# Kernel tuning notes

Measured on AMD Instinct MI355X. Metric: run time of the kernel, lower is better.

Reference implementation:

```python
import math
import jax, jax.numpy as jnp
import numpy as np

B, L, D_IN, H, NLAYER, FUT, MDIM = 16, 128, 8, 128, 2, 12, 2

def setup_inputs() -> dict:
    key = jax.random.key(0)
    ks = jax.random.split(key, 16)
    def rn(k, shape, scale=0.05):
        return jax.random.normal(k, shape, jnp.float32) * scale
    return {
        'history': jax.random.normal(ks[0], (B, L, D_IN), jnp.float32),
        'history_mask': jnp.ones((B, L), jnp.float32),
        'Wp': rn(ks[1], (D_IN, H)), 'bp': jnp.zeros((H,), jnp.float32),
        'We1': rn(ks[2], (NLAYER, 4, H)), 'be1': jnp.zeros((NLAYER, H), jnp.float32),
        'We2': rn(ks[3], (NLAYER, H, H)), 'be2': jnp.zeros((NLAYER, H), jnp.float32),
        'Wa1': rn(ks[4], (NLAYER, 3 * H, H)), 'ba1': jnp.zeros((NLAYER, H), jnp.float32),
        'wa2': rn(ks[5], (NLAYER, H)), 'ba2': jnp.zeros((NLAYER,), jnp.float32),
        'Wm1': rn(ks[6], (NLAYER, 2 * H, H)), 'bm1': jnp.zeros((NLAYER, H), jnp.float32),
        'Wm2': rn(ks[7], (NLAYER, H, H)), 'bm2': jnp.zeros((NLAYER, H), jnp.float32),
        'Wo1': rn(ks[8], (NLAYER, 2 * H, H)), 'bo1': jnp.zeros((NLAYER, H), jnp.float32),
        'Wo2': rn(ks[9], (NLAYER, H, H)), 'bo2': jnp.zeros((NLAYER, H), jnp.float32),
        'ln_g': jnp.ones((NLAYER, H), jnp.float32), 'ln_b': jnp.zeros((NLAYER, H), jnp.float32),
        'hg': jnp.ones((D_IN + H,), jnp.float32), 'hb': jnp.zeros((D_IN + H,), jnp.float32),
        'Wh1': rn(ks[10], (D_IN + H, H)), 'bh1': jnp.zeros((H,), jnp.float32),
        'Wh2': rn(ks[11], (H, FUT * MDIM)), 'bh2': jnp.zeros((FUT * MDIM,), jnp.float32),
    }

def _layer_norm(x, g, b):
    mu = jnp.mean(x, -1, keepdims=True)
    var = jnp.mean((x - mu) ** 2, -1, keepdims=True)
    return (x - mu) * jax.lax.rsqrt(var + 1e-5) * g + b

def _forward(history, history_mask, Wp, bp, We1, be1, We2, be2, Wa1, ba1, wa2, ba2,
             Wm1, bm1, Wm2, bm2, Wo1, bo1, Wo2, bo2, ln_g, ln_b, hg, hb, Wh1, bh1, Wh2, bh2):
    valid = history_mask > 0
    vm = valid.astype(jnp.float32)[..., None]
    ts = jnp.cumsum(jnp.maximum(history[..., 5], 0.0), axis=1)
    # edge features [B,L,L,4]: dist, dt/300, same_src, same_step
    lat, lon, src_flag = history[..., 0], history[..., 1], history[..., 6]
    dlat = lat[:, :, None] - lat[:, None, :]
    dlon = lon[:, :, None] - lon[:, None, :]
    dist = jnp.sqrt(dlat * dlat + dlon * dlon + 1e-8)
    dt = jnp.abs(ts[:, :, None] - ts[:, None, :]) / 300.0
    same_src = (src_flag[:, :, None] == src_flag[:, None, :]).astype(jnp.float32)
    same_step = jnp.broadcast_to(jnp.eye(L, dtype=jnp.float32), (B, L, L))
    edge_feat = jnp.stack([dist, dt, same_src, same_step], axis=-1)
    h = (history @ Wp + bp) * vm
    inv = 1.0 / math.sqrt(H)
    for l in range(NLAYER):
        eh = jax.nn.relu(edge_feat @ We1[l] + be1[l]) @ We2[l] + be2[l]  # [B,L,L,H]
        # att MLP on concat([src,dst,edge]) -> split first weight into blocks
        sa = h @ Wa1[l, :H]       # src term, varies over i
        da = h @ Wa1[l, H:2 * H]  # dst term, varies over j
        att_hid = jnp.tanh(sa[:, :, None, :] + da[:, None, :, :] + eh @ Wa1[l, 2 * H:] + ba1[l])
        att = (att_hid @ wa2[l] + ba2[l]) * inv  # [B,L,L]
        att = jnp.where(valid[:, None, :], att, -1e9)  # key invalid
        att = jnp.where(valid[:, :, None], att, -1e9)  # query invalid
        w = jax.nn.softmax(att, axis=-1)
        # msg MLP on concat([src, edge])
        msg = jax.nn.relu((h @ Wm1[l, :H])[:, :, None, :] + eh @ Wm1[l, H:] + bm1[l]) @ Wm2[l] + bm2[l]
        agg = jnp.einsum('bij,bijk->bik', w, msg)
        out = jax.nn.relu(h @ Wo1[l, :H] + agg @ Wo1[l, H:] + bo1[l]) @ Wo2[l] + bo2[l]
        h = _layer_norm(h + out, ln_g[l], ln_b[l]) * vm
    # decoder state: last valid step
    vc = jnp.clip(jnp.sum(history_mask, axis=1).astype(jnp.int32), 1, L)
    last = vc - 1
    bidx = jnp.arange(B)
    ds = jnp.concatenate([history[bidx, last], h[bidx, last]], axis=-1)
    x = _layer_norm(ds, hg, hb)
    pred = (jax.nn.relu(x @ Wh1 + bh1) @ Wh2 + bh2).reshape(B, FUT, MDIM)
    pred = jnp.nan_to_num(pred, nan=0.0, posinf=1e4, neginf=-1e4)
    return pred, h

def reference(history, history_mask, Wp, bp, We1, be1, We2, be2, Wa1, ba1, wa2, ba2,
              Wm1, bm1, Wm2, bm2, Wo1, bo1, Wo2, bo2, ln_g, ln_b, hg, hb, Wh1, bh1, Wh2, bh2):
    return _forward(history, history_mask, Wp, bp, We1, be1, We2, be2, Wa1, ba1, wa2, ba2,
                    Wm1, bm1, Wm2, bm2, Wo1, bo1, Wo2, bo2, ln_g, ln_b, hg, hb, Wh1, bh1, Wh2, bh2)
```

## Files before the change

### kernel.cpp

```cpp
#include <hip/hip_runtime.h>
#include <math.h>

#define BB 16
#define LL 128
#define D_IN 8
#define HH 128
#define NLAYER 2
#define FUT 12
#define MDIM 2

typedef __attribute__((ext_vector_type(8))) __bf16 bf16x8;
typedef __attribute__((ext_vector_type(8))) short short8v;
typedef __attribute__((ext_vector_type(4))) float f32x4;

#define MFMA_B16(A, B, C) __builtin_amdgcn_mfma_f32_16x16x32_bf16(A, B, C, 0, 0, 0)

static __device__ __forceinline__ short f2bf(float f) {
    union { float f; unsigned u; } v; v.f = f;
    unsigned r = v.u + 0x7FFFu + ((v.u >> 16) & 1u);
    return (short)(r >> 16);
}

static __device__ __forceinline__ float tanh_fast(float x) {
    float e = __expf(2.f * x);
    return 1.f - 2.f / (e + 1.f);
}

__global__ __launch_bounds__(256) void k_prep(const float* __restrict__ hist, const float* __restrict__ mask,
                                              const float* __restrict__ Wp, const float* __restrict__ bp,
                                              const float* __restrict__ We2, const float* __restrict__ be2,
                                              const float* __restrict__ Wa1, const float* __restrict__ ba1,
                                              const float* __restrict__ Wm1, const float* __restrict__ bm1,
                                              const float* __restrict__ Wo1, const float* __restrict__ Wm2,
                                              const float* __restrict__ Wo2,
                                              float* __restrict__ ts, float* __restrict__ h,
                                              short* __restrict__ AmT, short* __restrict__ MmT,
                                              float* __restrict__ ca, float* __restrict__ cm,
                                              short* __restrict__ WT4, short* __restrict__ WT3) {
    __shared__ float row[HH];
    __shared__ float pa[256], pm[256];
    const int bid = blockIdx.x, tid = threadIdx.x;
    const int NC = NLAYER * (HH + 1);
    if (bid < BB) {
        int b = bid;
        if (tid < LL) row[tid] = fmaxf(hist[(b * LL + tid) * D_IN + 5], 0.f);
        __syncthreads();
        for (int d = 1; d < LL; d <<= 1) {
            float add = (tid < LL && tid >= d) ? row[tid - d] : 0.f;
            __syncthreads();
            if (tid < LL) row[tid] += add;
            __syncthreads();
        }
        if (tid < LL) ts[b * LL + tid] = row[tid];
        int k = tid & (HH - 1);
        float wp_r[D_IN];
#pragma unroll
        for (int f = 0; f < D_IN; f++) wp_r[f] = Wp[f * HH + k];
        float bpk = bp[k];
        int jbase = tid >> 7;
        for (int e = 0; e < 64; e++) {
            int j = e * 2 + jbase;
            int bj = b * LL + j;
            const float* hr = hist + (size_t)bj * D_IN;
            float acc = bpk;
#pragma unroll
            for (int f = 0; f < D_IN; f++) acc += hr[f] * wp_r[f];
            h[(size_t)bj * HH + k] = acc * (mask[bj] > 0.f ? 1.f : 0.f);
        }
    } else if (bid < BB + NC) {
        int cb = bid - BB;
        int l = cb / (HH + 1);
        int p = cb % (HH + 1);
        const float* WaE = Wa1 + (size_t)(l * 3 * HH + 2 * HH) * HH;
        const float* WmE = Wm1 + (size_t)(l * 2 * HH + HH) * HH;
        int q = tid & 127, kh = tid >> 7;
        if (tid < HH) row[tid] = (p < HH) ? We2[(size_t)(l * HH + p) * HH + tid] : be2[l * HH + tid];
        __syncthreads();
        float a = 0.f, m = 0.f;
        int kbase = kh * 64;
#pragma unroll 4
        for (int k = 0; k < 64; k++) {
            float w = row[kbase + k];
            a += w * WaE[(size_t)(kbase + k) * HH + q];
            m += w * WmE[(size_t)(kbase + k) * HH + q];
        }
        pa[tid] = a;
        pm[tid] = m;
        __syncthreads();
        if (tid < HH) {
            a = pa[tid] + pa[128 + tid];
            m = pm[tid] + pm[128 + tid];
            if (p < HH) {
                AmT[(size_t)l * HH * HH + tid * HH + p] = f2bf(a);
                MmT[(size_t)l * HH * HH + tid * HH + p] = f2bf(m);
            } else {
                ca[l * HH + tid] = a + ba1[l * HH + tid];
                cm[l * HH + tid] = m + bm1[l * HH + tid];
            }
        }
    } else {
        int m7 = bid - BB - NC;
        int l = m7 / 7, m = m7 % 7;
        const float* src;
        switch (m) {
            case 0: src = Wa1 + (size_t)(l * 3 * HH) * HH; break;
            case 1: src = Wa1 + (size_t)(l * 3 * HH + HH) * HH; break;
            case 2: src = Wm1 + (size_t)(l * 2 * HH) * HH; break;
            case 3: src = Wo1 + (size_t)(l * 2 * HH) * HH; break;
            case 4: src = Wm2 + (size_t)l * HH * HH; break;
            case 5: src = Wo1 + (size_t)(l * 2 * HH + HH) * HH; break;
            default: src = Wo2 + (size_t)l * HH * HH; break;
        }
        short* dst = (m < 4) ? (WT4 + (size_t)(l * 4 + m) * HH * HH)
                             : (WT3 + (size_t)(l * 3 + (m - 4)) * HH * HH);
#pragma unroll 4
        for (int e = 0; e < 64; e++) {
            int idx = e * 256 + tid;
            int kk = idx >> 7;
            int c = idx & 127;
            dst[c * HH + kk] = f2bf(src[(size_t)kk * HH + c]);
        }
    }
}

__global__ __launch_bounds__(256) void k_pre(const float* __restrict__ h, const short* __restrict__ WT4,
                                             const float* __restrict__ ca, const float* __restrict__ cm,
                                             float* __restrict__ base_a, float* __restrict__ da,
                                             float* __restrict__ base_m, float* __restrict__ oa, int l) {
    __shared__ __align__(16) short hA[16][136];
    const int tid = threadIdx.x, lane = tid & 63, wv = tid >> 6;
    const int lo = lane & 15, g4 = lane >> 4;
    const int rt = blockIdx.x >> 1, half = blockIdx.x & 1;
    const int r0 = rt * 16;
    {
        int row = tid >> 4, cc = (tid & 15) * 8;
        const float* hr = h + (size_t)(r0 + row) * HH + cc;
        short8v pk;
#pragma unroll
        for (int e = 0; e < 8; e++) pk[e] = f2bf(hr[e]);
        *(short8v*)&hA[row][cc] = pk;
    }
    __syncthreads();
    bf16x8 af[4];
#pragma unroll
    for (int ks = 0; ks < 4; ks++)
        af[ks] = *(const bf16x8*)&hA[lo][ks * 32 + g4 * 8];
    const int mat = half * 2 + (wv & 1);
    const int ctbase = (wv >> 1) * 4;
    const short* Wl = WT4 + (size_t)(l * 4 + mat) * HH * HH;
    float* dst;
    const float* bias = nullptr;
    if (mat == 0) { dst = base_a; bias = ca + l * HH; }
    else if (mat == 1) dst = da;
    else if (mat == 2) { dst = base_m; bias = cm + l * HH; }
    else dst = oa;
#pragma unroll
    for (int cc2 = 0; cc2 < 4; cc2++) {
        int col = (ctbase + cc2) * 16 + lo;
        bf16x8 Bf[4];
#pragma unroll
        for (int ks = 0; ks < 4; ks++)
            Bf[ks] = *(const bf16x8*)(Wl + (size_t)col * HH + ks * 32 + g4 * 8);
        f32x4 acc = (f32x4){0.f, 0.f, 0.f, 0.f};
#pragma unroll
        for (int ks = 0; ks < 4; ks++) acc = MFMA_B16(af[ks], Bf[ks], acc);
        float bv = bias ? bias[col] : 0.f;
#pragma unroll
        for (int rg = 0; rg < 4; rg++)
            dst[(size_t)(r0 + g4 * 4 + rg) * HH + col] = acc[rg] + bv;
    }
}

__global__ __launch_bounds__(512) void k_attn(
    const float* __restrict__ hist, const float* __restrict__ mask, const float* __restrict__ ts,
    const float* __restrict__ base_a_g, const float* __restrict__ base_m_g, const float* __restrict__ da,
    const short* __restrict__ AmT, const short* __restrict__ MmT,
    const float* __restrict__ wa2, const float* __restrict__ ba2,
    const float* __restrict__ We1, const float* __restrict__ be1,
    float* __restrict__ v_out, int l) {
    __shared__ __align__(16) short t_lds[LL][LL];
    __shared__ __align__(16) float bufA[1024];
    __shared__ float w_lds[LL];
    __shared__ float val_s[LL];

    const int tid = threadIdx.x;
    const int lane = tid & 63;
    const int wv = tid >> 6;
    const int lo = lane & 15, g4 = lane >> 4;
    const int kq = wv * 16 + g4 * 4;
    const int bi = blockIdx.x, b = bi >> 7, i = bi & (LL - 1);

    const f32x4 ba4 = *(const f32x4*)(base_a_g + (size_t)bi * HH + kq);
    const f32x4 bm4 = *(const f32x4*)(base_m_g + (size_t)bi * HH + kq);
    const f32x4 wa4 = *(const f32x4*)(wa2 + l * HH + kq);
    const float ba2l = ba2[l];

    bf16x8 Bf[4];
#pragma unroll
    for (int ks = 0; ks < 4; ks++)
        Bf[ks] = *(const bf16x8*)(AmT + (size_t)l * HH * HH + (size_t)(wv * 16 + lo) * HH + ks * 32 + g4 * 8);

    {
        const float* We1l = We1 + l * 4 * HH;
        const float* be1l = be1 + l * HH;
        if (tid < 256) bufA[tid] = We1l[tid];
        else if (tid < 384) bufA[tid] = be1l[tid - 256];
        else bufA[tid] = be1l[tid - 384] + We1l[256 + (tid - 384)];
        if (tid < 128) {
            bufA[512 + tid] = We1l[384 + tid];
            val_s[tid] = mask[b * LL + tid];
        }
    }
    __syncthreads();

    {
        int jj = tid & (LL - 1);
        int q4 = tid >> 7;
        const float* hri = hist + (size_t)(b * LL + i) * D_IN;
        const float* hrj = hist + (size_t)(b * LL + jj) * D_IN;
        float dlat = hri[0] - hrj[0], dlon = hri[1] - hrj[1];
        float ea = sqrtf(dlat * dlat + dlon * dlon + 1e-8f);
        float eb = fabsf(ts[b * LL + i] - ts[b * LL + jj]) * (1.f / 300.f);
        const float* basep = bufA + ((hri[6] == hrj[6]) ? 384 : 256);
        char* trow = (char*)t_lds + jj * 256;
        int swz = (jj & 7) << 4;
        bool diag = (jj == i);
#pragma unroll
        for (int pass = 0; pass < 4; pass++) {
            int r0c = (q4 + pass * 4) * 8;
            f32x4 v0, v1;
            {
                f32x4 wa0 = *(const f32x4*)&bufA[r0c];
                f32x4 wb0 = *(const f32x4*)&bufA[128 + r0c];
                f32x4 bs0 = *(const f32x4*)&basep[r0c];
                v0 = wa0 * ea + wb0 * eb + bs0;
                f32x4 wa1 = *(const f32x4*)&bufA[r0c + 4];
                f32x4 wb1 = *(const f32x4*)&bufA[128 + r0c + 4];
                f32x4 bs1 = *(const f32x4*)&basep[r0c + 4];
                v1 = wa1 * ea + wb1 * eb + bs1;
            }
            if (diag) {
                v0 += *(const f32x4*)&bufA[512 + r0c];
                v1 += *(const f32x4*)&bufA[512 + r0c + 4];
            }
            bf16x8 pkb;
#pragma unroll
            for (int e = 0; e < 4; e++) {
                pkb[e] = (__bf16)fmaxf(v0[e], 0.f);
                pkb[4 + e] = (__bf16)fmaxf(v1[e], 0.f);
            }
            *(bf16x8*)(trow + ((r0c * 2) ^ swz)) = pkb;
        }
    }
    __syncthreads();

    const float* da_b = da + (size_t)(b * LL) * HH;
    const int rswz = (lo & 7) << 4;

#pragma unroll
    for (int jh = 0; jh < 2; jh++) {
        f32x4 acc[4];
#pragma unroll
        for (int m = 0; m < 4; m++) {
            int j0 = (jh * 4 + m) * 16 + lo;
            acc[m] = *(const f32x4*)(da_b + (size_t)j0 * HH + kq);
        }
#pragma unroll
        for (int ks = 0; ks < 4; ks++) {
            bf16x8 tf[4];
#pragma unroll
            for (int m = 0; m < 4; m++) {
                int row = (jh * 4 + m) * 16 + lo;
                tf[m] = *(const bf16x8*)((const char*)t_lds + row * 256 + ((ks * 64 + g4 * 16) ^ rswz));
            }
#pragma unroll
            for (int m = 0; m < 4; m++) acc[m] = MFMA_B16(Bf[ks], tf[m], acc[m]);
        }
#pragma unroll
        for (int m = 0; m < 4; m++) {
            f32x4 s = acc[m] + ba4;
            float p0 = tanh_fast(s[0]) * wa4[0];
            float p1 = tanh_fast(s[1]) * wa4[1];
            float p2 = tanh_fast(s[2]) * wa4[2];
            float p3 = tanh_fast(s[3]) * wa4[3];
            float p = (p0 + p1) + (p2 + p3);
            p += __shfl_xor(p, 16);
            p += __shfl_xor(p, 32);
            if (g4 == 0) bufA[wv * LL + (jh * 4 + m) * 16 + lo] = p;
        }
    }

#pragma unroll
    for (int ks = 0; ks < 4; ks++)
        Bf[ks] = *(const bf16x8*)(MmT + (size_t)l * HH * HH + (size_t)(wv * 16 + lo) * HH + ks * 32 + g4 * 8);
    __syncthreads();

    {
        const float inv = 0.08838834764831845f;
        float vi = val_s[i];
        float a0 = ba2l, a1 = ba2l;
#pragma unroll
        for (int w = 0; w < 8; w++) {
            a0 += bufA[w * LL + lane];
            a1 += bufA[w * LL + 64 + lane];
        }
        a0 *= inv; a1 *= inv;
        if (!(val_s[lane] > 0.f) || !(vi > 0.f)) a0 = -1e9f;
        if (!(val_s[64 + lane] > 0.f) || !(vi > 0.f)) a1 = -1e9f;
        float m = fmaxf(a0, a1);
#pragma unroll
        for (int d = 1; d < 64; d <<= 1) m = fmaxf(m, __shfl_xor(m, d));
        float e0 = __expf(a0 - m), e1 = __expf(a1 - m);
        float s = e0 + e1;
#pragma unroll
        for (int d = 1; d < 64; d <<= 1) s += __shfl_xor(s, d);
        float rs = 1.f / s;
        w_lds[lane] = e0 * rs;
        w_lds[64 + lane] = e1 * rs;
    }

    f32x4 macv = (f32x4){0.f, 0.f, 0.f, 0.f};
#pragma unroll
    for (int jh = 0; jh < 2; jh++) {
        f32x4 acc[4];
#pragma unroll
        for (int m = 0; m < 4; m++) acc[m] = (f32x4){0.f, 0.f, 0.f, 0.f};
#pragma unroll
        for (int ks = 0; ks < 4; ks++) {
            bf16x8 tf[4];
#pragma unroll
            for (int m = 0; m < 4; m++) {
                int row = (jh * 4 + m) * 16 + lo;
                tf[m] = *(const bf16x8*)((const char*)t_lds + row * 256 + ((ks * 64 + g4 * 16) ^ rswz));
            }
#pragma unroll
            for (int m = 0; m < 4; m++) acc[m] = MFMA_B16(Bf[ks], tf[m], acc[m]);
        }
#pragma unroll
        for (int m = 0; m < 4; m++) {
            float wj = w_lds[(jh * 4 + m) * 16 + lo];
            f32x4 mm = acc[m] + bm4;
#pragma unroll
            for (int rg = 0; rg < 4; rg++) mm[rg] = fmaxf(mm[rg], 0.f);
            macv += mm * wj;
        }
    }
#pragma unroll
    for (int rg = 0; rg < 4; rg++) {
        macv[rg] += __shfl_xor(macv[rg], 1);
        macv[rg] += __shfl_xor(macv[rg], 2);
        macv[rg] += __shfl_xor(macv[rg], 4);
        macv[rg] += __shfl_xor(macv[rg], 8);
    }
    if (lo == 0) *(f32x4*)(v_out + (size_t)bi * HH + kq) = macv;
}

__global__ __launch_bounds__(256) void k_post(
    const float* __restrict__ v, const float* __restrict__ oa_in, const float* __restrict__ h,
    const float* __restrict__ mask, const short* __restrict__ WT3,
    const float* __restrict__ bm2, const float* __restrict__ bo1, const float* __restrict__ bo2,
    const float* __restrict__ ln_g, const float* __restrict__ ln_b,
    float* __restrict__ hout, float* __restrict__ hcopy, int l,
    int do_pre, const short* __restrict__ WT4, const float* __restrict__ ca, const float* __restrict__ cm,
    float* __restrict__ base_a, float* __restrict__ da, float* __restrict__ base_m, float* __restrict__ oa_out,
    const float* __restrict__ hist, const float* __restrict__ hg, const float* __restrict__ hb,
    const float* __restrict__ Wh1, const float* __restrict__ bh1,
    const float* __restrict__ Wh2, const float* __restrict__ bh2, float* __restrict__ dec_out) {
    __shared__ __align__(16) short xA[16][136];
    __shared__ __align__(16) short iA[16][136];
    __shared__ float red[2][4][16];
    __shared__ float ln_row[HH];
    __shared__ float dec_x[D_IN + HH];
    const int tid = threadIdx.x, lane = tid & 63, wv = tid >> 6;
    const int lo = lane & 15, g4 = lane >> 4;
    const int r0 = blockIdx.x * 16;

    float oaR[2][4], hR[2][4], vmR[4];
    float bm2R[2], bo1R[2], bo2R[2], gR[2], bR[2];
#pragma unroll
    for (int ct = 0; ct < 2; ct++) {
        int c = wv * 32 + ct * 16 + lo;
        bm2R[ct] = bm2[l * HH + c];
        bo1R[ct] = bo1[l * HH + c];
        bo2R[ct] = bo2[l * HH + c];
        gR[ct] = ln_g[l * HH + c];
        bR[ct] = ln_b[l * HH + c];
    }
#pragma unroll
    for (int rg = 0; rg < 4; rg++) {
        int r = r0 + g4 * 4 + rg;
        vmR[rg] = mask[r];
#pragma unroll
        for (int ct = 0; ct < 2; ct++) {
            int c = wv * 32 + ct * 16 + lo;
            oaR[ct][rg] = oa_in[(size_t)r * HH + c];
            hR[ct][rg] = h[(size_t)r * HH + c];
        }
    }

    int lastRow = -1;
    if (hcopy) {
        float mv = (tid < LL) ? mask[(r0 >> 7) * LL + tid] : 0.f;
#pragma unroll
        for (int d = 1; d < 64; d <<= 1) mv += __shfl_xor(mv, d);
        if (lane == 0) red[0][wv][0] = mv;
    }

    {
        int row = tid >> 4, cc = (tid & 15) * 8;
        const float* vr = v + (size_t)(r0 + row) * HH + cc;
        short8v pk;
#pragma unroll
        for (int e = 0; e < 8; e++) pk[e] = f2bf(vr[e]);
        *(short8v*)&xA[row][cc] = pk;
    }
    __syncthreads();

    if (hcopy) {
        int vc = (int)(red[0][0][0] + red[0][1][0] + red[0][2][0] + red[0][3][0]);
        vc = min(max(vc, 1), LL);
        lastRow = (r0 & ~(LL - 1)) + vc - 1;
    }

    bf16x8 af[4], Bf[2][4];
    f32x4 acc[2];

    {
        const short* W = WT3 + (size_t)(l * 3 + 0) * HH * HH;
#pragma unroll
        for (int ks = 0; ks < 4; ks++) af[ks] = *(const bf16x8*)&xA[lo][ks * 32 + g4 * 8];
#pragma unroll
        for (int ct = 0; ct < 2; ct++) {
            int col = wv * 32 + ct * 16 + lo;
#pragma unroll
            for (int ks = 0; ks < 4; ks++)
                Bf[ct][ks] = *(const bf16x8*)(W + (size_t)col * HH + ks * 32 + g4 * 8);
        }
        acc[0] = (f32x4){0.f, 0.f, 0.f, 0.f};
        acc[1] = (f32x4){0.f, 0.f, 0.f, 0.f};
#pragma unroll
        for (int ks = 0; ks < 4; ks++) {
            acc[0] = MFMA_B16(af[ks], Bf[0][ks], acc[0]);
            acc[1] = MFMA_B16(af[ks], Bf[1][ks], acc[1]);
        }
#pragma unroll
        for (int ct = 0; ct < 2; ct++)
#pragma unroll
            for (int rg = 0; rg < 4; rg++)
                iA[g4 * 4 + rg][wv * 32 + ct * 16 + lo] = f2bf(acc[ct][rg] + bm2R[ct]);
    }
    __syncthreads();

    {
        const short* W = WT3 + (size_t)(l * 3 + 1) * HH * HH;
#pragma unroll
        for (int ks = 0; ks < 4; ks++) af[ks] = *(const bf16x8*)&iA[lo][ks * 32 + g4 * 8];
#pragma unroll
        for (int ct = 0; ct < 2; ct++) {
            int col = wv * 32 + ct * 16 + lo;
#pragma unroll
            for (int ks = 0; ks < 4; ks++)
                Bf[ct][ks] = *(const bf16x8*)(W + (size_t)col * HH + ks * 32 + g4 * 8);
        }
        acc[0] = (f32x4){0.f, 0.f, 0.f, 0.f};
        acc[1] = (f32x4){0.f, 0.f, 0.f, 0.f};
#pragma unroll
        for (int ks = 0; ks < 4; ks++) {
            acc[0] = MFMA_B16(af[ks], Bf[0][ks], acc[0]);
            acc[1] = MFMA_B16(af[ks], Bf[1][ks], acc[1]);
        }
        __syncthreads();
#pragma unroll
        for (int ct = 0; ct < 2; ct++)
#pragma unroll
            for (int rg = 0; rg < 4; rg++)
                xA[g4 * 4 + rg][wv * 32 + ct * 16 + lo] =
                    f2bf(fmaxf(acc[ct][rg] + oaR[ct][rg] + bo1R[ct], 0.f));
    }
    __syncthreads();

    float y[2][4];
    {
        const short* W = WT3 + (size_t)(l * 3 + 2) * HH * HH;
#pragma unroll
        for (int ks = 0; ks < 4; ks++) af[ks] = *(const bf16x8*)&xA[lo][ks * 32 + g4 * 8];
#pragma unroll
        for (int ct = 0; ct < 2; ct++) {
            int col = wv * 32 + ct * 16 + lo;
#pragma unroll
            for (int ks = 0; ks < 4; ks++)
                Bf[ct][ks] = *(const bf16x8*)(W + (size_t)col * HH + ks * 32 + g4 * 8);
        }
        acc[0] = (f32x4){0.f, 0.f, 0.f, 0.f};
        acc[1] = (f32x4){0.f, 0.f, 0.f, 0.f};
#pragma unroll
        for (int ks = 0; ks < 4; ks++) {
            acc[0] = MFMA_B16(af[ks], Bf[0][ks], acc[0]);
            acc[1] = MFMA_B16(af[ks], Bf[1][ks], acc[1]);
        }
#pragma unroll
        for (int ct = 0; ct < 2; ct++)
#pragma unroll
            for (int rg = 0; rg < 4; rg++)
                y[ct][rg] = acc[ct][rg] + bo2R[ct] + hR[ct][rg];
    }
#pragma unroll
    for (int rg = 0; rg < 4; rg++) {
        float s = y[0][rg] + y[1][rg];
        float s2 = y[0][rg] * y[0][rg] + y[1][rg] * y[1][rg];
#pragma unroll
        for (int d = 1; d < 16; d <<= 1) { s += __shfl_xor(s, d); s2 += __shfl_xor(s2, d); }
        if (lo == 0) {
            red[0][wv][g4 * 4 + rg] = s;
            red[1][wv][g4 * 4 + rg] = s2;
        }
    }
    __syncthreads();
#pragma unroll
    for (int rg = 0; rg < 4; rg++) {
        int rl = g4 * 4 + rg;
        float mu = (red[0][0][rl] + red[0][1][rl] + red[0][2][rl] + red[0][3][rl]) * (1.f / HH);
        float ex2 = (red[1][0][rl] + red[1][1][rl] + red[1][2][rl] + red[1][3][rl]) * (1.f / HH);
        float var = ex2 - mu * mu;
        float rs = rsqrtf(var + 1e-5f);
        float vm = vmR[rg] > 0.f ? 1.f : 0.f;
        int r = r0 + rl;
#pragma unroll
        for (int ct = 0; ct < 2; ct++) {
            int c = wv * 32 + ct * 16 + lo;
            float hv = ((y[ct][rg] - mu) * rs * gR[ct] + bR[ct]) * vm;
            hout[(size_t)r * HH + c] = hv;
            if (hcopy) hcopy[(size_t)r * HH + c] = hv;
            if (do_pre) xA[rl][c] = f2bf(hv);
            if (lastRow >= 0 && r == lastRow) ln_row[c] = hv;
        }
    }

    if (do_pre) {
        __syncthreads();
        bf16x8 af2[4];
#pragma unroll
        for (int ks = 0; ks < 4; ks++) af2[ks] = *(const bf16x8*)&xA[lo][ks * 32 + g4 * 8];
        int ln = l + 1;
        const short* Wl = WT4 + (size_t)(ln * 4 + wv) * HH * HH;
        float* dst;
        const float* bias = nullptr;
        if (wv == 0) { dst = base_a; bias = ca + ln * HH; }
        else if (wv == 1) dst = da;
        else if (wv == 2) { dst = base_m; bias = cm + ln * HH; }
        else dst = oa_out;
#pragma unroll
        for (int ct = 0; ct < 8; ct++) {
            int col = ct * 16 + lo;
            bf16x8 Bf2[4];
#pragma unroll
            for (int ks = 0; ks < 4; ks++)
                Bf2[ks] = *(const bf16x8*)(Wl + (size_t)col * HH + ks * 32 + g4 * 8);
            f32x4 a2 = (f32x4){0.f, 0.f, 0.f, 0.f};
#pragma unroll
            for (int ks = 0; ks < 4; ks++) a2 = MFMA_B16(af2[ks], Bf2[ks], a2);
            float bv = bias ? bias[col] : 0.f;
#pragma unroll
            for (int rg = 0; rg < 4; rg++)
                dst[(size_t)(r0 + g4 * 4 + rg) * HH + col] = a2[rg] + bv;
        }
    }

    if (hcopy && lastRow >= r0 && lastRow < r0 + 16) {
        const int N = D_IN + HH;
        __syncthreads();
        if (tid < D_IN) dec_x[tid] = hist[(size_t)lastRow * D_IN + tid];
        if (tid < HH) dec_x[D_IN + tid] = ln_row[tid];
        __syncthreads();
        float px = (tid < N) ? dec_x[tid] : 0.f;
        float px2 = px * px;
#pragma unroll
        for (int d = 1; d < 64; d <<= 1) { px += __shfl_xor(px, d); px2 += __shfl_xor(px2, d); }
        if (lane == 0) { red[0][wv][0] = px; red[1][wv][0] = px2; }
        __syncthreads();
        float mu = (red[0][0][0] + red[0][1][0] + red[0][2][0] + red[0][3][0]) / (float)N;
        float ex2 = (red[1][0][0] + red[1][1][0] + red[1][2][0] + red[1][3][0]) / (float)N;
        float var = ex2 - mu * mu;
        float rs = rsqrtf(var + 1e-5f);
        if (tid < N) dec_x[tid] = (dec_x[tid] - mu) * rs * hg[tid] + hb[tid];
        __syncthreads();
        if (tid < HH) {
            float a = bh1[tid];
            for (int f = 0; f < N; f++) a += dec_x[f] * Wh1[(size_t)f * HH + tid];
            ln_row[tid] = fmaxf(a, 0.f);
        }
        __syncthreads();
        if (tid < FUT * MDIM) {
            float o = bh2[tid];
            for (int k = 0; k < HH; k++) o += ln_row[k] * Wh2[(size_t)k * FUT * MDIM + tid];
            if (isnan(o)) o = 0.f;
            else if (isinf(o)) o = (o > 0.f) ? 1e4f : -1e4f;
            dec_out[(r0 >> 7) * FUT * MDIM + tid] = o;
        }
    }
}

extern "C" void kernel_launch(void* const* d_in, const int* in_sizes, int n_in,
                              void* d_out, int out_size, void* d_ws, size_t ws_size,
                              hipStream_t stream) {
    const float* hist = (const float*)d_in[0];
    const float* mask = (const float*)d_in[1];
    const float* Wp  = (const float*)d_in[2];
    const float* bp  = (const float*)d_in[3];
    const float* We1 = (const float*)d_in[4];
    const float* be1 = (const float*)d_in[5];
    const float* We2 = (const float*)d_in[6];
    const float* be2 = (const float*)d_in[7];
    const float* Wa1 = (const float*)d_in[8];
    const float* ba1 = (const float*)d_in[9];
    const float* wa2 = (const float*)d_in[10];
    const float* ba2 = (const float*)d_in[11];
    const float* Wm1 = (const float*)d_in[12];
    const float* bm1 = (const float*)d_in[13];
    const float* Wm2 = (const float*)d_in[14];
    const float* bm2 = (const float*)d_in[15];
    const float* Wo1 = (const float*)d_in[16];
    const float* bo1 = (const float*)d_in[17];
    const float* Wo2 = (const float*)d_in[18];
    const float* bo2 = (const float*)d_in[19];
    const float* ln_g = (const float*)d_in[20];
    const float* ln_b = (const float*)d_in[21];
    const float* hg  = (const float*)d_in[22];
    const float* hb  = (const float*)d_in[23];
    const float* Wh1 = (const float*)d_in[24];
    const float* bh1 = (const float*)d_in[25];
    const float* Wh2 = (const float*)d_in[26];
    const float* bh2 = (const float*)d_in[27];
    float* out = (float*)d_out;

    float* ws = (float*)d_ws;
    float* ts_w   = ws; ws += BB * LL;
    float* h_w    = ws; ws += BB * LL * HH;
    float* da_w   = ws; ws += BB * LL * HH;
    float* ba_w   = ws; ws += BB * LL * HH;
    float* bm_w   = ws; ws += BB * LL * HH;
    float* oa_w   = ws; ws += BB * LL * HH;
    float* v_w    = ws; ws += BB * LL * HH;
    float* ca_w   = ws; ws += NLAYER * HH;
    float* cm_w   = ws; ws += NLAYER * HH;
    short* AmT_w  = (short*)ws; ws += NLAYER * HH * HH / 2;
    short* MmT_w  = (short*)ws; ws += NLAYER * HH * HH / 2;
    short* WT4_w  = (short*)ws; ws += NLAYER * 4 * HH * HH / 2;
    short* WT3_w  = (short*)ws; ws += NLAYER * 3 * HH * HH / 2;

    const int NPREP = BB + NLAYER * (HH + 1) + NLAYER * 7;
    k_prep<<<NPREP, 256, 0, stream>>>(hist, mask, Wp, bp, We2, be2, Wa1, ba1, Wm1, bm1,
                                      Wo1, Wm2, Wo2, ts_w, h_w, AmT_w, MmT_w, ca_w, cm_w, WT4_w, WT3_w);
    k_pre<<<BB * LL / 16 * 2, 256, 0, stream>>>(h_w, WT4_w, ca_w, cm_w, ba_w, da_w, bm_w, oa_w, 0);
    for (int l = 0; l < NLAYER; l++) {
        k_attn<<<BB * LL, 512, 0, stream>>>(hist, mask, ts_w, ba_w, bm_w, da_w, AmT_w, MmT_w,
                                            wa2, ba2, We1, be1, v_w, l);
        int do_pre = (l < NLAYER - 1) ? 1 : 0;
        float* hcopy = (l == NLAYER - 1) ? (out + BB * FUT * MDIM) : nullptr;
        k_post<<<BB * LL / 16, 256, 0, stream>>>(v_w, oa_w, h_w, mask, WT3_w, bm2, bo1, bo2,
                                                 ln_g, ln_b, h_w, hcopy, l,
                                                 do_pre, WT4_w, ca_w, cm_w, ba_w, da_w, bm_w, oa_w,
                                                 hist, hg, hb, Wh1, bh1, Wh2, bh2, out);
    }
}
```

Before: 258.5 us.

## Widen k_pre and k_post to 512 threads and prefetch weight fragments

k_pre and k_post now run 8 waves per 16-row block instead of 4, with each wave owning one 16-column tile (k_post) or one matrix half (k_pre). All B-fragments are loaded from global memory up front, before the LDS staging and barriers, so the weight loads overlap them. k_prep stages the history rows and mask in shared memory instead of re-reading global memory inside the loop. The cost is higher register pressure from holding all weight fragments, plus larger cross-wave reductions for the layer norm.

```diff
diff --git a/kernel.cpp b/kernel.cpp
--- a/kernel.cpp
+++ b/kernel.cpp
@@ -11,6 +11,7 @@
 
 typedef __attribute__((ext_vector_type(8))) __bf16 bf16x8;
 typedef __attribute__((ext_vector_type(8))) short short8v;
+typedef __attribute__((ext_vector_type(4))) short short4v;
 typedef __attribute__((ext_vector_type(4))) float f32x4;
 
 #define MFMA_B16(A, B, C) __builtin_amdgcn_mfma_f32_16x16x32_bf16(A, B, C, 0, 0, 0)
@@ -39,11 +40,16 @@
                                               short* __restrict__ WT4, short* __restrict__ WT3) {
     __shared__ float row[HH];
     __shared__ float pa[256], pm[256];
+    __shared__ float hrow[LL * D_IN];
     const int bid = blockIdx.x, tid = threadIdx.x;
     const int NC = NLAYER * (HH + 1);
     if (bid < BB) {
         int b = bid;
-        if (tid < LL) row[tid] = fmaxf(hist[(b * LL + tid) * D_IN + 5], 0.f);
+#pragma unroll
+        for (int e = 0; e < 4; e++) hrow[e * 256 + tid] = hist[(size_t)b * LL * D_IN + e * 256 + tid];
+        if (tid < LL) pa[tid] = mask[b * LL + tid];
+        __syncthreads();
+        if (tid < LL) row[tid] = fmaxf(hrow[tid * D_IN + 5], 0.f);
         __syncthreads();
         for (int d = 1; d < LL; d <<= 1) {
             float add = (tid < LL && tid >= d) ? row[tid - d] : 0.f;
@@ -60,12 +66,11 @@
         int jbase = tid >> 7;
         for (int e = 0; e < 64; e++) {
             int j = e * 2 + jbase;
-            int bj = b * LL + j;
-            const float* hr = hist + (size_t)bj * D_IN;
+            const float* hr = &hrow[j * D_IN];
             float acc = bpk;
 #pragma unroll
             for (int f = 0; f < D_IN; f++) acc += hr[f] * wp_r[f];
-            h[(size_t)bj * HH + k] = acc * (mask[bj] > 0.f ? 1.f : 0.f);
+            h[(size_t)(b * LL + j) * HH + k] = acc * (pa[j] > 0.f ? 1.f : 0.f);
         }
     } else if (bid < BB + NC) {
         int cb = bid - BB;
@@ -123,31 +128,39 @@
     }
 }
 
-__global__ __launch_bounds__(256) void k_pre(const float* __restrict__ h, const short* __restrict__ WT4,
+__global__ __launch_bounds__(512) void k_pre(const float* __restrict__ h, const short* __restrict__ WT4,
                                              const float* __restrict__ ca, const float* __restrict__ cm,
                                              float* __restrict__ base_a, float* __restrict__ da,
                                              float* __restrict__ base_m, float* __restrict__ oa, int l) {
     __shared__ __align__(16) short hA[16][136];
     const int tid = threadIdx.x, lane = tid & 63, wv = tid >> 6;
     const int lo = lane & 15, g4 = lane >> 4;
-    const int rt = blockIdx.x >> 1, half = blockIdx.x & 1;
-    const int r0 = rt * 16;
+    const int r0 = blockIdx.x * 16;
+    const int mat = wv >> 1, colh = wv & 1;
+
+    const short* Wl = WT4 + (size_t)(l * 4 + mat) * HH * HH;
+    bf16x8 Bf[4][4];
+#pragma unroll
+    for (int t = 0; t < 4; t++) {
+        int col = (colh * 4 + t) * 16 + lo;
+#pragma unroll
+        for (int ks = 0; ks < 4; ks++)
+            Bf[t][ks] = *(const bf16x8*)(Wl + (size_t)col * HH + ks * 32 + g4 * 8);
+    }
+
     {
-        int row = tid >> 4, cc = (tid & 15) * 8;
+        int row = tid >> 5, cc = (tid & 31) * 4;
         const float* hr = h + (size_t)(r0 + row) * HH + cc;
-        short8v pk;
-#pragma unroll
-        for (int e = 0; e < 8; e++) pk[e] = f2bf(hr[e]);
-        *(short8v*)&hA[row][cc] = pk;
+        short4v pk;
+#pragma unroll
+        for (int e = 0; e < 4; e++) pk[e] = f2bf(hr[e]);
+        *(short4v*)&hA[row][cc] = pk;
     }
     __syncthreads();
     bf16x8 af[4];
 #pragma unroll
     for (int ks = 0; ks < 4; ks++)
         af[ks] = *(const bf16x8*)&hA[lo][ks * 32 + g4 * 8];
-    const int mat = half * 2 + (wv & 1);
-    const int ctbase = (wv >> 1) * 4;
-    const short* Wl = WT4 + (size_t)(l * 4 + mat) * HH * HH;
     float* dst;
     const float* bias = nullptr;
     if (mat == 0) { dst = base_a; bias = ca + l * HH; }
@@ -155,15 +168,11 @@
     else if (mat == 2) { dst = base_m; bias = cm + l * HH; }
     else dst = oa;
 #pragma unroll
-    for (int cc2 = 0; cc2 < 4; cc2++) {
-        int col = (ctbase + cc2) * 16 + lo;
-        bf16x8 Bf[4];
-#pragma unroll
-        for (int ks = 0; ks < 4; ks++)
-            Bf[ks] = *(const bf16x8*)(Wl + (size_t)col * HH + ks * 32 + g4 * 8);
+    for (int t = 0; t < 4; t++) {
+        int col = (colh * 4 + t) * 16 + lo;
         f32x4 acc = (f32x4){0.f, 0.f, 0.f, 0.f};
 #pragma unroll
-        for (int ks = 0; ks < 4; ks++) acc = MFMA_B16(af[ks], Bf[ks], acc);
+        for (int ks = 0; ks < 4; ks++) acc = MFMA_B16(af[ks], Bf[t][ks], acc);
         float bv = bias ? bias[col] : 0.f;
 #pragma unroll
         for (int rg = 0; rg < 4; rg++)
@@ -355,7 +364,7 @@
     if (lo == 0) *(f32x4*)(v_out + (size_t)bi * HH + kq) = macv;
 }
 
-__global__ __launch_bounds__(256) void k_post(
+__global__ __launch_bounds__(512) void k_post(
     const float* __restrict__ v, const float* __restrict__ oa_in, const float* __restrict__ h,
     const float* __restrict__ mask, const short* __restrict__ WT3,
     const float* __restrict__ bm2, const float* __restrict__ bo1, const float* __restrict__ bo2,
@@ -368,34 +377,36 @@
     const float* __restrict__ Wh2, const float* __restrict__ bh2, float* __restrict__ dec_out) {
     __shared__ __align__(16) short xA[16][136];
     __shared__ __align__(16) short iA[16][136];
-    __shared__ float red[2][4][16];
+    __shared__ float red[2][8][16];
     __shared__ float ln_row[HH];
     __shared__ float dec_x[D_IN + HH];
     const int tid = threadIdx.x, lane = tid & 63, wv = tid >> 6;
     const int lo = lane & 15, g4 = lane >> 4;
     const int r0 = blockIdx.x * 16;
-
-    float oaR[2][4], hR[2][4], vmR[4];
-    float bm2R[2], bo1R[2], bo2R[2], gR[2], bR[2];
-#pragma unroll
-    for (int ct = 0; ct < 2; ct++) {
-        int c = wv * 32 + ct * 16 + lo;
-        bm2R[ct] = bm2[l * HH + c];
-        bo1R[ct] = bo1[l * HH + c];
-        bo2R[ct] = bo2[l * HH + c];
-        gR[ct] = ln_g[l * HH + c];
-        bR[ct] = ln_b[l * HH + c];
-    }
+    const int c = wv * 16 + lo;
+
+    bf16x8 BfA[4], BfB[4], BfC[4];
+    {
+        const short* WA = WT3 + (size_t)(l * 3 + 0) * HH * HH;
+        const short* WB = WT3 + (size_t)(l * 3 + 1) * HH * HH;
+        const short* WC = WT3 + (size_t)(l * 3 + 2) * HH * HH;
+#pragma unroll
+        for (int ks = 0; ks < 4; ks++) {
+            BfA[ks] = *(const bf16x8*)(WA + (size_t)c * HH + ks * 32 + g4 * 8);
+            BfB[ks] = *(const bf16x8*)(WB + (size_t)c * HH + ks * 32 + g4 * 8);
+            BfC[ks] = *(const bf16x8*)(WC + (size_t)c * HH + ks * 32 + g4 * 8);
+        }
+    }
+
+    float oaR[4], hR[4], vmR[4];
+    const float bm2R = bm2[l * HH + c], bo1R = bo1[l * HH + c], bo2R = bo2[l * HH + c];
+    const float gR = ln_g[l * HH + c], bR = ln_b[l * HH + c];
 #pragma unroll
     for (int rg = 0; rg < 4; rg++) {
         int r = r0 + g4 * 4 + rg;
         vmR[rg] = mask[r];
-#pragma unroll
-        for (int ct = 0; ct < 2; ct++) {
-            int c = wv * 32 + ct * 16 + lo;
-            oaR[ct][rg] = oa_in[(size_t)r * HH + c];
-            hR[ct][rg] = h[(size_t)r * HH + c];
-        }
+        oaR[rg] = oa_in[(size_t)r * HH + c];
+        hR[rg] = h[(size_t)r * HH + c];
     }
 
     int lastRow = -1;
@@ -407,107 +418,59 @@
     }
 
     {
-        int row = tid >> 4, cc = (tid & 15) * 8;
+        int row = tid >> 5, cc = (tid & 31) * 4;
         const float* vr = v + (size_t)(r0 + row) * HH + cc;
-        short8v pk;
-#pragma unroll
-        for (int e = 0; e < 8; e++) pk[e] = f2bf(vr[e]);
-        *(short8v*)&xA[row][cc] = pk;
+        short4v pk;
+#pragma unroll
+        for (int e = 0; e < 4; e++) pk[e] = f2bf(vr[e]);
+        *(short4v*)&xA[row][cc] = pk;
     }
     __syncthreads();
 
     if (hcopy) {
-        int vc = (int)(red[0][0][0] + red[0][1][0] + red[0][2][0] + red[0][3][0]);
+        float vcs = 0.f;
+#pragma unroll
+        for (int w = 0; w < 8; w++) vcs += red[0][w][0];
+        int vc = (int)vcs;
         vc = min(max(vc, 1), LL);
         lastRow = (r0 & ~(LL - 1)) + vc - 1;
     }
 
-    bf16x8 af[4], Bf[2][4];
-    f32x4 acc[2];
-
-    {
-        const short* W = WT3 + (size_t)(l * 3 + 0) * HH * HH;
-#pragma unroll
-        for (int ks = 0; ks < 4; ks++) af[ks] = *(const bf16x8*)&xA[lo][ks * 32 + g4 * 8];
-#pragma unroll
-        for (int ct = 0; ct < 2; ct++) {
-            int col = wv * 32 + ct * 16 + lo;
-#pragma unroll
-            for (int ks = 0; ks < 4; ks++)
-                Bf[ct][ks] = *(const bf16x8*)(W + (size_t)col * HH + ks * 32 + g4 * 8);
-        }
-        acc[0] = (f32x4){0.f, 0.f, 0.f, 0.f};
-        acc[1] = (f32x4){0.f, 0.f, 0.f, 0.f};
-#pragma unroll
-        for (int ks = 0; ks < 4; ks++) {
-            acc[0] = MFMA_B16(af[ks], Bf[0][ks], acc[0]);
-            acc[1] = MFMA_B16(af[ks], Bf[1][ks], acc[1]);
-        }
-#pragma unroll
-        for (int ct = 0; ct < 2; ct++)
-#pragma unroll
-            for (int rg = 0; rg < 4; rg++)
-                iA[g4 * 4 + rg][wv * 32 + ct * 16 + lo] = f2bf(acc[ct][rg] + bm2R[ct]);
-    }
-    __syncthreads();
-
-    {
-        const short* W = WT3 + (size_t)(l * 3 + 1) * HH * HH;
-#pragma unroll
-        for (int ks = 0; ks < 4; ks++) af[ks] = *(const bf16x8*)&iA[lo][ks * 32 + g4 * 8];
-#pragma unroll
-        for (int ct = 0; ct < 2; ct++) {
-            int col = wv * 32 + ct * 16 + lo;
-#pragma unroll
-            for (int ks = 0; ks < 4; ks++)
-                Bf[ct][ks] = *(const bf16x8*)(W + (size_t)col * HH + ks * 32 + g4 * 8);
-        }
-        acc[0] = (f32x4){0.f, 0.f, 0.f, 0.f};
-        acc[1] = (f32x4){0.f, 0.f, 0.f, 0.f};
-#pragma unroll
-        for (int ks = 0; ks < 4; ks++) {
-            acc[0] = MFMA_B16(af[ks], Bf[0][ks], acc[0]);
-            acc[1] = MFMA_B16(af[ks], Bf[1][ks], acc[1]);
-        }
-        __syncthreads();
-#pragma unroll
-        for (int ct = 0; ct < 2; ct++)
-#pragma unroll
-            for (int rg = 0; rg < 4; rg++)
-                xA[g4 * 4 + rg][wv * 32 + ct * 16 + lo] =
-                    f2bf(fmaxf(acc[ct][rg] + oaR[ct][rg] + bo1R[ct], 0.f));
-    }
-    __syncthreads();
-
-    float y[2][4];
-    {
-        const short* W = WT3 + (size_t)(l * 3 + 2) * HH * HH;
-#pragma unroll
-        for (int ks = 0; ks < 4; ks++) af[ks] = *(const bf16x8*)&xA[lo][ks * 32 + g4 * 8];
-#pragma unroll
-        for (int ct = 0; ct < 2; ct++) {
-            int col = wv * 32 + ct * 16 + lo;
-#pragma unroll
-            for (int ks = 0; ks < 4; ks++)
-                Bf[ct][ks] = *(const bf16x8*)(W + (size_t)col * HH + ks * 32 + g4 * 8);
-        }
-        acc[0] = (f32x4){0.f, 0.f, 0.f, 0.f};
-        acc[1] = (f32x4){0.f, 0.f, 0.f, 0.f};
-#pragma unroll
-        for (int ks = 0; ks < 4; ks++) {
-            acc[0] = MFMA_B16(af[ks], Bf[0][ks], acc[0]);
-            acc[1] = MFMA_B16(af[ks], Bf[1][ks], acc[1]);
-        }
-#pragma unroll
-        for (int ct = 0; ct < 2; ct++)
-#pragma unroll
-            for (int rg = 0; rg < 4; rg++)
-                y[ct][rg] = acc[ct][rg] + bo2R[ct] + hR[ct][rg];
-    }
+    bf16x8 af[4];
+    f32x4 acc;
+
+#pragma unroll
+    for (int ks = 0; ks < 4; ks++) af[ks] = *(const bf16x8*)&xA[lo][ks * 32 + g4 * 8];
+    acc = (f32x4){0.f, 0.f, 0.f, 0.f};
+#pragma unroll
+    for (int ks = 0; ks < 4; ks++) acc = MFMA_B16(af[ks], BfA[ks], acc);
+#pragma unroll
+    for (int rg = 0; rg < 4; rg++) iA[g4 * 4 + rg][c] = f2bf(acc[rg] + bm2R);
+    __syncthreads();
+
+#pragma unroll
+    for (int ks = 0; ks < 4; ks++) af[ks] = *(const bf16x8*)&iA[lo][ks * 32 + g4 * 8];
+    acc = (f32x4){0.f, 0.f, 0.f, 0.f};
+#pragma unroll
+    for (int ks = 0; ks < 4; ks++) acc = MFMA_B16(af[ks], BfB[ks], acc);
+#pragma unroll
+    for (int rg = 0; rg < 4; rg++)
+        xA[g4 * 4 + rg][c] = f2bf(fmaxf(acc[rg] + oaR[rg] + bo1R, 0.f));
+    __syncthreads();
+
+    float y[4];
+#pragma unroll
+    for (int ks = 0; ks < 4; ks++) af[ks] = *(const bf16x8*)&xA[lo][ks * 32 + g4 * 8];
+    acc = (f32x4){0.f, 0.f, 0.f, 0.f};
+#pragma unroll
+    for (int ks = 0; ks < 4; ks++) acc = MFMA_B16(af[ks], BfC[ks], acc);
+#pragma unroll
+    for (int rg = 0; rg < 4; rg++) y[rg] = acc[rg] + bo2R + hR[rg];
+
 #pragma unroll
     for (int rg = 0; rg < 4; rg++) {
-        float s = y[0][rg] + y[1][rg];
-        float s2 = y[0][rg] * y[0][rg] + y[1][rg] * y[1][rg];
+        float s = y[rg];
+        float s2 = y[rg] * y[rg];
 #pragma unroll
         for (int d = 1; d < 16; d <<= 1) { s += __shfl_xor(s, d); s2 += __shfl_xor(s2, d); }
         if (lo == 0) {
@@ -519,50 +482,54 @@
 #pragma unroll
     for (int rg = 0; rg < 4; rg++) {
         int rl = g4 * 4 + rg;
-        float mu = (red[0][0][rl] + red[0][1][rl] + red[0][2][rl] + red[0][3][rl]) * (1.f / HH);
-        float ex2 = (red[1][0][rl] + red[1][1][rl] + red[1][2][rl] + red[1][3][rl]) * (1.f / HH);
+        float mu = 0.f, ex2 = 0.f;
+#pragma unroll
+        for (int w = 0; w < 8; w++) { mu += red[0][w][rl]; ex2 += red[1][w][rl]; }
+        mu *= (1.f / HH);
+        ex2 *= (1.f / HH);
         float var = ex2 - mu * mu;
         float rs = rsqrtf(var + 1e-5f);
         float vm = vmR[rg] > 0.f ? 1.f : 0.f;
         int r = r0 + rl;
-#pragma unroll
-        for (int ct = 0; ct < 2; ct++) {
-            int c = wv * 32 + ct * 16 + lo;
-            float hv = ((y[ct][rg] - mu) * rs * gR[ct] + bR[ct]) * vm;
-            hout[(size_t)r * HH + c] = hv;
-            if (hcopy) hcopy[(size_t)r * HH + c] = hv;
-            if (do_pre) xA[rl][c] = f2bf(hv);
-            if (lastRow >= 0 && r == lastRow) ln_row[c] = hv;
-        }
+        float hv = ((y[rg] - mu) * rs * gR + bR) * vm;
+        hout[(size_t)r * HH + c] = hv;
+        if (hcopy) hcopy[(size_t)r * HH + c] = hv;
+        if (do_pre) xA[rl][c] = f2bf(hv);
+        if (lastRow >= 0 && r == lastRow) ln_row[c] = hv;
     }
 
     if (do_pre) {
+        int ln = l + 1;
+        int mat = wv >> 1, colh = wv & 1;
+        const short* Wl = WT4 + (size_t)(ln * 4 + mat) * HH * HH;
+        bf16x8 Bf2[4][4];
+#pragma unroll
+        for (int t = 0; t < 4; t++) {
+            int col2 = (colh * 4 + t) * 16 + lo;
+#pragma unroll
+            for (int ks = 0; ks < 4; ks++)
+                Bf2[t][ks] = *(const bf16x8*)(Wl + (size_t)col2 * HH + ks * 32 + g4 * 8);
+        }
         __syncthreads();
         bf16x8 af2[4];
 #pragma unroll
         for (int ks = 0; ks < 4; ks++) af2[ks] = *(const bf16x8*)&xA[lo][ks * 32 + g4 * 8];
-        int ln = l + 1;
-        const short* Wl = WT4 + (size_t)(ln * 4 + wv) * HH * HH;
         float* dst;
         const float* bias = nullptr;
-        if (wv == 0) { dst = base_a; bias = ca + ln * HH; }
-        else if (wv == 1) dst = da;
-        else if (wv == 2) { dst = base_m; bias = cm + ln * HH; }
+        if (mat == 0) { dst = base_a; bias = ca + ln * HH; }
+        else if (mat == 1) dst = da;
+        else if (mat == 2) { dst = base_m; bias = cm + ln * HH; }
         else dst = oa_out;
 #pragma unroll
-        for (int ct = 0; ct < 8; ct++) {
-            int col = ct * 16 + lo;
-            bf16x8 Bf2[4];
-#pragma unroll
-            for (int ks = 0; ks < 4; ks++)
-                Bf2[ks] = *(const bf16x8*)(Wl + (size_t)col * HH + ks * 32 + g4 * 8);
+        for (int t = 0; t < 4; t++) {
+            int col2 = (colh * 4 + t) * 16 + lo;
             f32x4 a2 = (f32x4){0.f, 0.f, 0.f, 0.f};
 #pragma unroll
-            for (int ks = 0; ks < 4; ks++) a2 = MFMA_B16(af2[ks], Bf2[ks], a2);
-            float bv = bias ? bias[col] : 0.f;
+            for (int ks = 0; ks < 4; ks++) a2 = MFMA_B16(af2[ks], Bf2[t][ks], a2);
+            float bv = bias ? bias[col2] : 0.f;
 #pragma unroll
             for (int rg = 0; rg < 4; rg++)
-                dst[(size_t)(r0 + g4 * 4 + rg) * HH + col] = a2[rg] + bv;
+                dst[(size_t)(r0 + g4 * 4 + rg) * HH + col2] = a2[rg] + bv;
         }
     }
 
@@ -578,8 +545,11 @@
         for (int d = 1; d < 64; d <<= 1) { px += __shfl_xor(px, d); px2 += __shfl_xor(px2, d); }
         if (lane == 0) { red[0][wv][0] = px; red[1][wv][0] = px2; }
         __syncthreads();
-        float mu = (red[0][0][0] + red[0][1][0] + red[0][2][0] + red[0][3][0]) / (float)N;
-        float ex2 = (red[1][0][0] + red[1][1][0] + red[1][2][0] + red[1][3][0]) / (float)N;
+        float mu = 0.f, ex2 = 0.f;
+#pragma unroll
+        for (int w = 0; w < 8; w++) { mu += red[0][w][0]; ex2 += red[1][w][0]; }
+        mu /= (float)N;
+        ex2 /= (float)N;
         float var = ex2 - mu * mu;
         float rs = rsqrtf(var + 1e-5f);
         if (tid < N) dec_x[tid] = (dec_x[tid] - mu) * rs * hg[tid] + hb[tid];
@@ -651,13 +621,13 @@
     const int NPREP = BB + NLAYER * (HH + 1) + NLAYER * 7;
     k_prep<<<NPREP, 256, 0, stream>>>(hist, mask, Wp, bp, We2, be2, Wa1, ba1, Wm1, bm1,
                                       Wo1, Wm2, Wo2, ts_w, h_w, AmT_w, MmT_w, ca_w, cm_w, WT4_w, WT3_w);
-    k_pre<<<BB * LL / 16 * 2, 256, 0, stream>>>(h_w, WT4_w, ca_w, cm_w, ba_w, da_w, bm_w, oa_w, 0);
+    k_pre<<<BB * LL / 16, 512, 0, stream>>>(h_w, WT4_w, ca_w, cm_w, ba_w, da_w, bm_w, oa_w, 0);
     for (int l = 0; l < NLAYER; l++) {
         k_attn<<<BB * LL, 512, 0, stream>>>(hist, mask, ts_w, ba_w, bm_w, da_w, AmT_w, MmT_w,
                                             wa2, ba2, We1, be1, v_w, l);
         int do_pre = (l < NLAYER - 1) ? 1 : 0;
         float* hcopy = (l == NLAYER - 1) ? (out + BB * FUT * MDIM) : nullptr;
-        k_post<<<BB * LL / 16, 256, 0, stream>>>(v_w, oa_w, h_w, mask, WT3_w, bm2, bo1, bo2,
+        k_post<<<BB * LL / 16, 512, 0, stream>>>(v_w, oa_w, h_w, mask, WT3_w, bm2, bo1, bo2,
                                                  ln_g, ln_b, h_w, hcopy, l,
                                                  do_pre, WT4_w, ca_w, cm_w, ba_w, da_w, bm_w, oa_w,
                                                  hist, hg, hb, Wh1, bh1, Wh2, bh2, out);
```

New measurement: 256.0 us. Within noise of the previous version (-1.0%).
